# Optimization experiments

Measured on AMD Instinct MI355X. Metric: run time of the kernel, lower is better.

## Reference

```python
import jax, jax.numpy as jnp
import numpy as np

N_EMBD = 1024
N_HEAD = 16
HEAD_DIM = 64


def setup_inputs() -> dict:
    key = jax.random.key(0)
    ks = jax.random.split(key, 5)
    x = jax.random.normal(ks[0], (4, 2048, N_EMBD), dtype=jnp.float32)
    # qkv_proj: Linear(n_embd, 3*n_embd) -- torch weight is [out, in]
    W_qkv = jax.random.normal(ks[1], (3 * N_EMBD, N_EMBD), dtype=jnp.float32) * 0.02
    b_qkv = jnp.zeros((3 * N_EMBD,), dtype=jnp.float32)
    W_out = jax.random.normal(ks[2], (N_EMBD, N_EMBD), dtype=jnp.float32) * 0.02
    b_out = jnp.zeros((N_EMBD,), dtype=jnp.float32)
    return {"x": x, "W_qkv": W_qkv, "b_qkv": b_qkv, "W_out": W_out, "b_out": b_out}


def reference(x, W_qkv, b_qkv, W_out, b_out):
    B, S, C = x.shape
    scale = 1.0 / np.sqrt(HEAD_DIM)
    qkv = jnp.einsum('bsc,oc->bso', x, W_qkv) + b_qkv  # [B,S,3C]
    q, k, v = jnp.split(qkv, 3, axis=-1)
    # [B,S,C] -> [B,H,S,Dh]
    def to_heads(t):
        return t.reshape(B, S, N_HEAD, HEAD_DIM).transpose(0, 2, 1, 3)
    q, k, v = to_heads(q), to_heads(k), to_heads(v)
    scores = jnp.einsum('bhqd,bhkd->bhqk', q, k) * scale  # [B,H,S,S]
    causal = jnp.tril(jnp.ones((S, S), dtype=bool))
    scores = jnp.where(causal[None, None], scores, -jnp.inf)
    weights = jax.nn.softmax(scores.astype(jnp.float32), axis=-1).astype(q.dtype)
    y = jnp.einsum('bhqk,bhkd->bhqd', weights, v)  # [B,H,S,Dh]
    y = y.transpose(0, 2, 1, 3).reshape(B, S, C)
    return jnp.einsum('bsc,oc->bso', y, W_out) + b_out
```

## Files before the change

### kernel.cpp

```cpp
#include <hip/hip_runtime.h>
#include <stdint.h>
#include <stddef.h>

typedef __attribute__((ext_vector_type(8))) short short8;
typedef __attribute__((ext_vector_type(4))) float f32x4;
typedef __attribute__((ext_vector_type(16))) float f32x16;
typedef __attribute__((ext_vector_type(4))) unsigned short ushort4v;
typedef __attribute__((ext_vector_type(4))) unsigned int uint4v;

#define SEQ   2048
#define NH    16
#define BATCH 4
#define GK    1024

__device__ __forceinline__ unsigned short f2bf(float f) {
  union { float f; unsigned int u; } v; v.f = f;
  unsigned int u = v.u;
  u += 0x7fffu + ((u >> 16) & 1u);
  return (unsigned short)(u >> 16);
}

__device__ __forceinline__ unsigned cvtpk_bf16(float lo, float hi) {
  unsigned r;
  asm("v_cvt_pk_bf16_f32 %0, %1, %2" : "=v"(r) : "v"(lo), "v"(hi));
  return r;
}

__device__ __forceinline__ void plswap(unsigned &x, unsigned &y) {
#if __has_builtin(__builtin_amdgcn_permlane32_swap)
  auto r = __builtin_amdgcn_permlane32_swap((int)x, (int)y, false, false);
  x = (unsigned)r[0]; y = (unsigned)r[1];
#else
  const unsigned sx = (unsigned)__shfl_xor((int)x, 32);
  const unsigned sy = (unsigned)__shfl_xor((int)y, 32);
  const bool hi = (threadIdx.x & 63) >= 32;
  const unsigned nx = hi ? sy : x;
  const unsigned ny = hi ? y : sx;
  x = nx; y = ny;
#endif
}

__device__ __forceinline__ void gload16(const unsigned short* g, unsigned short* l) {
  __builtin_amdgcn_global_load_lds(
      (const __attribute__((address_space(1))) unsigned int*)g,
      (__attribute__((address_space(3))) unsigned int*)l, 16, 0, 0);
}

__global__ void cvt_bf16(const float* __restrict__ src, unsigned short* __restrict__ dst, int n4) {
  int i = blockIdx.x * blockDim.x + threadIdx.x;
  const int stride = gridDim.x * blockDim.x;
  for (; i < n4; i += stride) {
    const float4 v = reinterpret_cast<const float4*>(src)[i];
    ushort4v o;
    o[0] = f2bf(v.x); o[1] = f2bf(v.y); o[2] = f2bf(v.z); o[3] = f2bf(v.w);
    reinterpret_cast<ushort4v*>(dst)[i] = o;
  }
}

template<int MODE>
__global__ __launch_bounds__(256, 2)
void gemm_bt(const unsigned short* __restrict__ A,
             const unsigned short* __restrict__ Bw,
             const float* __restrict__ bias,
             unsigned short* __restrict__ q_ws,
             unsigned short* __restrict__ k_ws,
             unsigned short* __restrict__ v_ws,
             float* __restrict__ fout,
             int N)
{
  __shared__ __attribute__((aligned(16))) unsigned short As[128 * 64];
  __shared__ __attribute__((aligned(16))) unsigned short Bs[128 * 64];

  const int t = threadIdx.x;
  const int w = t >> 6, lane = t & 63;
  const int g = lane >> 4, c = lane & 15;
  const int wrow = w >> 1, wcol = w & 1;
  const int m0 = blockIdx.y * 128;
  const int n0 = blockIdx.x * 128;

  const int r8 = lane >> 3;
  const int cgs = (lane & 7) ^ r8;

  const f32x4 fz = {0.f, 0.f, 0.f, 0.f};
  f32x4 acc[4][4];
#pragma unroll
  for (int i = 0; i < 4; ++i)
#pragma unroll
    for (int j = 0; j < 4; ++j) acc[i][j] = fz;

  for (int ks = 0; ks < GK; ks += 64) {
    __syncthreads();
#pragma unroll
    for (int i = 0; i < 4; ++i) {
      const int RB = (i * 4 + w) * 8;
      gload16(A + (size_t)(m0 + RB + r8) * GK + ks + cgs * 8, &As[RB * 64]);
      gload16(Bw + (size_t)(n0 + RB + r8) * GK + ks + cgs * 8, &Bs[RB * 64]);
    }
    __syncthreads();
#pragma unroll
    for (int kk = 0; kk < 2; ++kk) {
      short8 af[4], bfr[4];
#pragma unroll
      for (int mi = 0; mi < 4; ++mi) {
        const int row = wrow * 64 + mi * 16 + c;
        af[mi] = *reinterpret_cast<const short8*>(&As[row * 64 + (((kk * 4 + g) ^ (row & 7)) << 3)]);
      }
#pragma unroll
      for (int ni = 0; ni < 4; ++ni) {
        const int row = wcol * 64 + ni * 16 + c;
        bfr[ni] = *reinterpret_cast<const short8*>(&Bs[row * 64 + (((kk * 4 + g) ^ (row & 7)) << 3)]);
      }
#pragma unroll
      for (int mi = 0; mi < 4; ++mi)
#pragma unroll
        for (int ni = 0; ni < 4; ++ni)
          acc[mi][ni] = __builtin_amdgcn_mfma_f32_16x16x32_bf16(af[mi], bfr[ni], acc[mi][ni], 0, 0, 0);
    }
  }

  if (MODE == 0) {
    const int sec = n0 >> 10;
    unsigned short* dst = (sec == 0) ? q_ws : ((sec == 1) ? k_ws : v_ws);
    const float qsc = (sec == 0) ? (0.125f * 1.44269504f) : 1.0f;
#pragma unroll
    for (int ni = 0; ni < 4; ++ni) {
      const int n = n0 + wcol * 64 + ni * 16 + c;
      const float bb = bias[n];
      const int hh = (n & 1023) >> 6;
      const int d = n & 63;
#pragma unroll
      for (int mi = 0; mi < 4; ++mi) {
#pragma unroll
        for (int r = 0; r < 4; ++r) {
          const int m = m0 + wrow * 64 + mi * 16 + g * 4 + r;
          const int b = m >> 11, s = m & 2047;
          const float val = (acc[mi][ni][r] + bb) * qsc;
          dst[((size_t)((b * NH + hh) * SEQ + s) << 6) + d] = f2bf(val);
        }
      }
    }
  } else {
#pragma unroll
    for (int ni = 0; ni < 4; ++ni) {
      const int n = n0 + wcol * 64 + ni * 16 + c;
      const float bb = bias[n];
#pragma unroll
      for (int mi = 0; mi < 4; ++mi) {
#pragma unroll
        for (int r = 0; r < 4; ++r) {
          const int m = m0 + wrow * 64 + mi * 16 + g * 4 + r;
          fout[(size_t)m * N + n] = acc[mi][ni][r] + bb;
        }
      }
    }
  }
}

__global__ __launch_bounds__(256)
void transpose_v(const unsigned short* __restrict__ v, unsigned short* __restrict__ vt) {
  __shared__ unsigned short T[64][72];
  const int t = threadIdx.x;
  const int bh = blockIdx.y, s0 = blockIdx.x * 64;
  const unsigned short* src = v + ((size_t)bh * SEQ + s0) * 64;
#pragma unroll
  for (int rep = 0; rep < 2; ++rep) {
    const int u = rep * 256 + t;
    const int sr = u >> 3, cg = u & 7;
    const short8 x = *reinterpret_cast<const short8*>(src + (size_t)sr * 64 + cg * 8);
    *reinterpret_cast<short8*>(&T[sr][cg * 8]) = x;
  }
  __syncthreads();
  unsigned short* dst = vt + (size_t)bh * 64 * SEQ + s0;
#pragma unroll
  for (int rep = 0; rep < 2; ++rep) {
    const int u = rep * 256 + t;
    const int d = u >> 3, sc8 = u & 7;
    short8 x;
#pragma unroll
    for (int j = 0; j < 8; ++j) x[j] = (short)T[sc8 * 8 + j][d];
    *reinterpret_cast<short8*>(dst + (size_t)d * SEQ + sc8 * 8) = x;
  }
}

__global__ __launch_bounds__(512, 4)
void attn_fwd4(const unsigned short* __restrict__ q_ws,
               const unsigned short* __restrict__ k_ws,
               const unsigned short* __restrict__ vt_ws,
               unsigned short* __restrict__ y_ws)
{
  __shared__ __attribute__((aligned(16))) unsigned short Ks[2][64 * 64];
  __shared__ __attribute__((aligned(16))) unsigned short Vs[2][64 * 64];

  const int t = threadIdx.x;
  const int w = t >> 6, lane = t & 63;
  const int ql = lane & 31, hi = lane >> 5;
  const int bh = blockIdx.y, b = bh >> 4, h = bh & 15;
  const int jt = (blockIdx.y >= 32) ? (7 - (int)blockIdx.x) : (int)blockIdx.x;
  const int wq0 = jt * 256 + w * 32;
  const int nkt = 4 * jt + 4;

  const int s_row = t >> 3, s_cg = t & 7;
  const int so = s_row * 64 + ((s_cg ^ (s_row & 7)) << 3);

  const unsigned short* kbase = k_ws + (size_t)bh * SEQ * 64;
  const unsigned short* vbase = vt_ws + (size_t)bh * 64 * SEQ;

  short8 rk, rv;
  auto stage_issue = [&](int kt) {
    rk = *reinterpret_cast<const short8*>(kbase + (size_t)kt * 4096 + s_row * 64 + s_cg * 8);
    rv = *reinterpret_cast<const short8*>(vbase + (size_t)s_row * SEQ + kt * 64 + s_cg * 8);
  };
  auto stage_write = [&](int bi) {
    *reinterpret_cast<short8*>(&Ks[bi][so]) = rk;
    *reinterpret_cast<short8*>(&Vs[bi][so]) = rv;
  };

  const unsigned short* qr = q_ws + ((size_t)bh * SEQ + (wq0 + ql)) * 64;
  short8 qf[4];
#pragma unroll
  for (int ks = 0; ks < 4; ++ks)
    qf[ks] = *reinterpret_cast<const short8*>(qr + ks * 16 + hi * 8);

  f32x16 o0, o1;
#pragma unroll
  for (int i = 0; i < 16; ++i) { o0[i] = 0.f; o1[i] = 0.f; }
  float m_run = -1e30f, lsum = 0.f;

  stage_issue(0);
  stage_write(0);

#pragma unroll 1
  for (int kt = 0; kt < nkt; ++kt) {
    const bool more = (kt + 1) < nkt;
    if (more) stage_issue(kt + 1);
    __syncthreads();
    const int cur = kt & 1;
    const int kt64 = kt * 64;

    if (kt64 <= wq0 + 31) {
      short8 kfl[4], kfh[4];
#pragma unroll
      for (int ks = 0; ks < 4; ++ks) {
        kfl[ks] = *reinterpret_cast<const short8*>(
            &Ks[cur][ql * 64 + (((2 * ks + hi) ^ (ql & 7)) << 3)]);
        kfh[ks] = *reinterpret_cast<const short8*>(
            &Ks[cur][(32 + ql) * 64 + (((2 * ks + hi) ^ (ql & 7)) << 3)]);
      }
      f32x16 s0, s1;
#pragma unroll
      for (int i = 0; i < 16; ++i) { s0[i] = 0.f; s1[i] = 0.f; }
      __builtin_amdgcn_s_setprio(1);
#pragma unroll
      for (int ks = 0; ks < 4; ++ks) {
        s0 = __builtin_amdgcn_mfma_f32_32x32x16_bf16(kfl[ks], qf[ks], s0, 0, 0, 0);
        s1 = __builtin_amdgcn_mfma_f32_32x32x16_bf16(kfh[ks], qf[ks], s1, 0, 0, 0);
      }
      __builtin_amdgcn_s_setprio(0);
      if (kt64 + 63 > wq0) {
        const int gq = wq0 + ql;
#pragma unroll
        for (int r = 0; r < 16; ++r) {
          const int krow = (r & 3) + 8 * (r >> 2) + 4 * hi;
          if (kt64 + krow > gq)      s0[r] = -1e30f;
          if (kt64 + 32 + krow > gq) s1[r] = -1e30f;
        }
      }
      float tm = -1e30f;
#pragma unroll
      for (int r = 0; r < 16; ++r) tm = fmaxf(tm, fmaxf(s0[r], s1[r]));
      tm = fmaxf(tm, __shfl_xor(tm, 32));
      if (__any(tm > m_run + 10.0f)) {
        const float m_new = fmaxf(m_run, tm);
        const float al = __builtin_amdgcn_exp2f(m_run - m_new);
        m_run = m_new;
        lsum *= al;
#pragma unroll
        for (int r = 0; r < 16; ++r) {
          const int qq = (r & 3) + 8 * (r >> 2) + 4 * hi;
          const float ar = __shfl(al, qq);
          o0[r] *= ar; o1[r] *= ar;
        }
      }
      float psum = 0.f;
      unsigned W[16];
#pragma unroll
      for (int half = 0; half < 2; ++half) {
#pragma unroll
        for (int gr = 0; gr < 4; ++gr) {
          const float v0 = (half ? s1[gr * 4 + 0] : s0[gr * 4 + 0]) - m_run;
          const float v1 = (half ? s1[gr * 4 + 1] : s0[gr * 4 + 1]) - m_run;
          const float v2 = (half ? s1[gr * 4 + 2] : s0[gr * 4 + 2]) - m_run;
          const float v3 = (half ? s1[gr * 4 + 3] : s0[gr * 4 + 3]) - m_run;
          const float p0 = __builtin_amdgcn_exp2f(v0);
          const float p1 = __builtin_amdgcn_exp2f(v1);
          const float p2 = __builtin_amdgcn_exp2f(v2);
          const float p3 = __builtin_amdgcn_exp2f(v3);
          psum += (p0 + p1) + (p2 + p3);
          W[half * 8 + 2 * gr]     = cvtpk_bf16(p0, p1);
          W[half * 8 + 2 * gr + 1] = cvtpk_bf16(p2, p3);
        }
      }
      lsum += psum;
      short8 pa[4];
#pragma unroll
      for (int q4 = 0; q4 < 4; ++q4) {
        unsigned a0 = W[q4 * 4 + 0], a1 = W[q4 * 4 + 2];
        unsigned b0 = W[q4 * 4 + 1], b1 = W[q4 * 4 + 3];
        plswap(a0, a1);
        plswap(b0, b1);
        uint4v pk; pk[0] = a0; pk[1] = b0; pk[2] = a1; pk[3] = b1;
        pa[q4] = __builtin_bit_cast(short8, pk);
      }
      __builtin_amdgcn_s_setprio(1);
#pragma unroll
      for (int ks = 0; ks < 4; ++ks) {
        const short8 vfl = *reinterpret_cast<const short8*>(
            &Vs[cur][ql * 64 + (((2 * ks + hi) ^ (ql & 7)) << 3)]);
        const short8 vfh = *reinterpret_cast<const short8*>(
            &Vs[cur][(32 + ql) * 64 + (((2 * ks + hi) ^ (ql & 7)) << 3)]);
        o0 = __builtin_amdgcn_mfma_f32_32x32x16_bf16(pa[ks], vfl, o0, 0, 0, 0);
        o1 = __builtin_amdgcn_mfma_f32_32x32x16_bf16(pa[ks], vfh, o1, 0, 0, 0);
      }
      __builtin_amdgcn_s_setprio(0);
    }
    if (more) stage_write((kt + 1) & 1);
  }

  lsum += __shfl_xor(lsum, 32);
  const float linv = 1.f / lsum;
#pragma unroll
  for (int r = 0; r < 16; ++r) {
    const int qq = (r & 3) + 8 * (r >> 2) + 4 * hi;
    const float lr = __shfl(linv, qq);
    const size_t rowo = ((size_t)b * SEQ + (wq0 + qq)) * 1024 + h * 64;
    y_ws[rowo + ql]      = f2bf(o0[r] * lr);
    y_ws[rowo + 32 + ql] = f2bf(o1[r] * lr);
  }
}

extern "C" void kernel_launch(void* const* d_in, const int* in_sizes, int n_in,
                              void* d_out, int out_size, void* d_ws, size_t ws_size,
                              hipStream_t stream)
{
  (void)in_sizes; (void)n_in; (void)out_size; (void)ws_size;
  const float* x     = (const float*)d_in[0];
  const float* W_qkv = (const float*)d_in[1];
  const float* b_qkv = (const float*)d_in[2];
  const float* W_out = (const float*)d_in[3];
  const float* b_out = (const float*)d_in[4];
  float* out = (float*)d_out;

  unsigned short* ws      = (unsigned short*)d_ws;
  unsigned short* x_bf    = ws;
  unsigned short* wqkv_bf = x_bf    + (size_t)8192 * 1024;
  unsigned short* wout_bf = wqkv_bf + (size_t)3072 * 1024;
  unsigned short* q_ws    = wout_bf + (size_t)1024 * 1024;
  unsigned short* k_ws    = q_ws    + (size_t)64 * SEQ * 64;
  unsigned short* v_ws    = k_ws    + (size_t)64 * SEQ * 64;
  unsigned short* y_ws    = v_ws    + (size_t)64 * SEQ * 64;
  unsigned short* vt_ws   = x_bf;

  cvt_bf16<<<2048, 256, 0, stream>>>(x,     x_bf,    (8192 * 1024) / 4);
  cvt_bf16<<<1024, 256, 0, stream>>>(W_qkv, wqkv_bf, (3072 * 1024) / 4);
  cvt_bf16<<<512,  256, 0, stream>>>(W_out, wout_bf, (1024 * 1024) / 4);

  gemm_bt<0><<<dim3(24, 64), 256, 0, stream>>>(x_bf, wqkv_bf, b_qkv, q_ws, k_ws, v_ws, nullptr, 3072);
  transpose_v<<<dim3(SEQ / 64, 64), 256, 0, stream>>>(v_ws, vt_ws);
  attn_fwd4<<<dim3(8, 64), 512, 0, stream>>>(q_ws, k_ws, vt_ws, y_ws);
  gemm_bt<1><<<dim3(8, 64), 256, 0, stream>>>(y_ws, wout_bf, b_out, nullptr, nullptr, nullptr, out, 1024);
}
```

Before: 180.9 us.

## Software-pipeline attention PV with QK, async LDS loads, fuse conversions

The attention kernel now stages K/V tiles with direct global-to-LDS loads and triple-buffers V. It also defers each tile's P·V MFMA to the next iteration so it overlaps with the following QK^T and softmax, with a tail step after the loop. The three fp32-to-bf16 conversion launches are merged into one kernel, and the GEMM launch bound is raised to three blocks per CU. The goals are to hide LDS staging latency, improve MFMA/VALU overlap and cut launch overhead, at the cost of more LDS, register pressure from the GEMM occupancy hint, and branchier conversion code.

```diff
diff --git a/kernel.cpp b/kernel.cpp
--- a/kernel.cpp
+++ b/kernel.cpp
@@ -46,11 +46,16 @@
       (__attribute__((address_space(3))) unsigned int*)l, 16, 0, 0);
 }
 
-__global__ void cvt_bf16(const float* __restrict__ src, unsigned short* __restrict__ dst, int n4) {
+__global__ void cvt_all(const float* __restrict__ x, const float* __restrict__ wqkv,
+                        const float* __restrict__ wout, unsigned short* __restrict__ dst) {
+  const int N1 = (8192 * 1024) / 4, N2 = (3072 * 1024) / 4, N3 = (1024 * 1024) / 4;
   int i = blockIdx.x * blockDim.x + threadIdx.x;
   const int stride = gridDim.x * blockDim.x;
-  for (; i < n4; i += stride) {
-    const float4 v = reinterpret_cast<const float4*>(src)[i];
+  for (; i < N1 + N2 + N3; i += stride) {
+    float4 v;
+    if (i < N1)            v = reinterpret_cast<const float4*>(x)[i];
+    else if (i < N1 + N2)  v = reinterpret_cast<const float4*>(wqkv)[i - N1];
+    else                   v = reinterpret_cast<const float4*>(wout)[i - N1 - N2];
     ushort4v o;
     o[0] = f2bf(v.x); o[1] = f2bf(v.y); o[2] = f2bf(v.z); o[3] = f2bf(v.w);
     reinterpret_cast<ushort4v*>(dst)[i] = o;
@@ -58,7 +63,7 @@
 }
 
 template<int MODE>
-__global__ __launch_bounds__(256, 2)
+__global__ __launch_bounds__(256, 3)
 void gemm_bt(const unsigned short* __restrict__ A,
              const unsigned short* __restrict__ Bw,
              const float* __restrict__ bias,
@@ -183,13 +188,13 @@
 }
 
 __global__ __launch_bounds__(512, 4)
-void attn_fwd4(const unsigned short* __restrict__ q_ws,
+void attn_fwd6(const unsigned short* __restrict__ q_ws,
                const unsigned short* __restrict__ k_ws,
                const unsigned short* __restrict__ vt_ws,
                unsigned short* __restrict__ y_ws)
 {
   __shared__ __attribute__((aligned(16))) unsigned short Ks[2][64 * 64];
-  __shared__ __attribute__((aligned(16))) unsigned short Vs[2][64 * 64];
+  __shared__ __attribute__((aligned(16))) unsigned short Vs[3][64 * 64];
 
   const int t = threadIdx.x;
   const int w = t >> 6, lane = t & 63;
@@ -199,20 +204,15 @@
   const int wq0 = jt * 256 + w * 32;
   const int nkt = 4 * jt + 4;
 
-  const int s_row = t >> 3, s_cg = t & 7;
-  const int so = s_row * 64 + ((s_cg ^ (s_row & 7)) << 3);
+  const int s_row = t >> 3;
+  const int s_swz = (t & 7) ^ (s_row & 7);
 
   const unsigned short* kbase = k_ws + (size_t)bh * SEQ * 64;
   const unsigned short* vbase = vt_ws + (size_t)bh * 64 * SEQ;
 
-  short8 rk, rv;
-  auto stage_issue = [&](int kt) {
-    rk = *reinterpret_cast<const short8*>(kbase + (size_t)kt * 4096 + s_row * 64 + s_cg * 8);
-    rv = *reinterpret_cast<const short8*>(vbase + (size_t)s_row * SEQ + kt * 64 + s_cg * 8);
-  };
-  auto stage_write = [&](int bi) {
-    *reinterpret_cast<short8*>(&Ks[bi][so]) = rk;
-    *reinterpret_cast<short8*>(&Vs[bi][so]) = rv;
+  auto stage = [&](int kt, int kb, int vb) {
+    gload16(kbase + (size_t)kt * 4096 + s_row * 64 + s_swz * 8, &Ks[kb][w * 512]);
+    gload16(vbase + (size_t)s_row * SEQ + kt * 64 + s_swz * 8, &Vs[vb][w * 512]);
   };
 
   const unsigned short* qr = q_ws + ((size_t)bh * SEQ + (wq0 + ql)) * 64;
@@ -225,37 +225,50 @@
 #pragma unroll
   for (int i = 0; i < 16; ++i) { o0[i] = 0.f; o1[i] = 0.f; }
   float m_run = -1e30f, lsum = 0.f;
-
-  stage_issue(0);
-  stage_write(0);
+  short8 pa[4];
+
+  stage(0, 0, 0);
 
 #pragma unroll 1
   for (int kt = 0; kt < nkt; ++kt) {
-    const bool more = (kt + 1) < nkt;
-    if (more) stage_issue(kt + 1);
     __syncthreads();
+    if (kt + 1 < nkt) stage(kt + 1, (kt + 1) & 1, (kt + 1) % 3);
     const int cur = kt & 1;
+    const int pvb = (kt + 2) % 3;
     const int kt64 = kt * 64;
-
-    if (kt64 <= wq0 + 31) {
-      short8 kfl[4], kfh[4];
-#pragma unroll
-      for (int ks = 0; ks < 4; ++ks) {
-        kfl[ks] = *reinterpret_cast<const short8*>(
-            &Ks[cur][ql * 64 + (((2 * ks + hi) ^ (ql & 7)) << 3)]);
-        kfh[ks] = *reinterpret_cast<const short8*>(
-            &Ks[cur][(32 + ql) * 64 + (((2 * ks + hi) ^ (ql & 7)) << 3)]);
-      }
-      f32x16 s0, s1;
+    const bool act  = (kt64 <= wq0 + 31);
+    const bool actp = (kt > 0) && (kt64 - 64 <= wq0 + 31);
+
+    f32x16 s0, s1;
+    if (act) {
 #pragma unroll
       for (int i = 0; i < 16; ++i) { s0[i] = 0.f; s1[i] = 0.f; }
       __builtin_amdgcn_s_setprio(1);
 #pragma unroll
       for (int ks = 0; ks < 4; ++ks) {
-        s0 = __builtin_amdgcn_mfma_f32_32x32x16_bf16(kfl[ks], qf[ks], s0, 0, 0, 0);
-        s1 = __builtin_amdgcn_mfma_f32_32x32x16_bf16(kfh[ks], qf[ks], s1, 0, 0, 0);
+        const short8 kfl = *reinterpret_cast<const short8*>(
+            &Ks[cur][ql * 64 + (((2 * ks + hi) ^ (ql & 7)) << 3)]);
+        const short8 kfh = *reinterpret_cast<const short8*>(
+            &Ks[cur][(32 + ql) * 64 + (((2 * ks + hi) ^ (ql & 7)) << 3)]);
+        s0 = __builtin_amdgcn_mfma_f32_32x32x16_bf16(kfl, qf[ks], s0, 0, 0, 0);
+        s1 = __builtin_amdgcn_mfma_f32_32x32x16_bf16(kfh, qf[ks], s1, 0, 0, 0);
       }
       __builtin_amdgcn_s_setprio(0);
+    }
+    if (actp) {
+      __builtin_amdgcn_s_setprio(1);
+#pragma unroll
+      for (int ks = 0; ks < 4; ++ks) {
+        const short8 vfl = *reinterpret_cast<const short8*>(
+            &Vs[pvb][ql * 64 + (((2 * ks + hi) ^ (ql & 7)) << 3)]);
+        const short8 vfh = *reinterpret_cast<const short8*>(
+            &Vs[pvb][(32 + ql) * 64 + (((2 * ks + hi) ^ (ql & 7)) << 3)]);
+        o0 = __builtin_amdgcn_mfma_f32_32x32x16_bf16(pa[ks], vfl, o0, 0, 0, 0);
+        o1 = __builtin_amdgcn_mfma_f32_32x32x16_bf16(pa[ks], vfh, o1, 0, 0, 0);
+      }
+      __builtin_amdgcn_s_setprio(0);
+    }
+    if (act) {
       if (kt64 + 63 > wq0) {
         const int gq = wq0 + ql;
 #pragma unroll
@@ -301,7 +314,6 @@
         }
       }
       lsum += psum;
-      short8 pa[4];
 #pragma unroll
       for (int q4 = 0; q4 < 4; ++q4) {
         unsigned a0 = W[q4 * 4 + 0], a1 = W[q4 * 4 + 2];
@@ -311,19 +323,22 @@
         uint4v pk; pk[0] = a0; pk[1] = b0; pk[2] = a1; pk[3] = b1;
         pa[q4] = __builtin_bit_cast(short8, pk);
       }
-      __builtin_amdgcn_s_setprio(1);
-#pragma unroll
-      for (int ks = 0; ks < 4; ++ks) {
-        const short8 vfl = *reinterpret_cast<const short8*>(
-            &Vs[cur][ql * 64 + (((2 * ks + hi) ^ (ql & 7)) << 3)]);
-        const short8 vfh = *reinterpret_cast<const short8*>(
-            &Vs[cur][(32 + ql) * 64 + (((2 * ks + hi) ^ (ql & 7)) << 3)]);
-        o0 = __builtin_amdgcn_mfma_f32_32x32x16_bf16(pa[ks], vfl, o0, 0, 0, 0);
-        o1 = __builtin_amdgcn_mfma_f32_32x32x16_bf16(pa[ks], vfh, o1, 0, 0, 0);
-      }
-      __builtin_amdgcn_s_setprio(0);
-    }
-    if (more) stage_write((kt + 1) & 1);
+    }
+  }
+
+  if ((nkt - 1) * 64 <= wq0 + 31) {
+    const int pvb = (nkt - 1) % 3;
+    __builtin_amdgcn_s_setprio(1);
+#pragma unroll
+    for (int ks = 0; ks < 4; ++ks) {
+      const short8 vfl = *reinterpret_cast<const short8*>(
+          &Vs[pvb][ql * 64 + (((2 * ks + hi) ^ (ql & 7)) << 3)]);
+      const short8 vfh = *reinterpret_cast<const short8*>(
+          &Vs[pvb][(32 + ql) * 64 + (((2 * ks + hi) ^ (ql & 7)) << 3)]);
+      o0 = __builtin_amdgcn_mfma_f32_32x32x16_bf16(pa[ks], vfl, o0, 0, 0, 0);
+      o1 = __builtin_amdgcn_mfma_f32_32x32x16_bf16(pa[ks], vfh, o1, 0, 0, 0);
+    }
+    __builtin_amdgcn_s_setprio(0);
   }
 
   lsum += __shfl_xor(lsum, 32);
@@ -360,12 +375,10 @@
   unsigned short* y_ws    = v_ws    + (size_t)64 * SEQ * 64;
   unsigned short* vt_ws   = x_bf;
 
-  cvt_bf16<<<2048, 256, 0, stream>>>(x,     x_bf,    (8192 * 1024) / 4);
-  cvt_bf16<<<1024, 256, 0, stream>>>(W_qkv, wqkv_bf, (3072 * 1024) / 4);
-  cvt_bf16<<<512,  256, 0, stream>>>(W_out, wout_bf, (1024 * 1024) / 4);
+  cvt_all<<<2048, 256, 0, stream>>>(x, W_qkv, W_out, x_bf);
 
   gemm_bt<0><<<dim3(24, 64), 256, 0, stream>>>(x_bf, wqkv_bf, b_qkv, q_ws, k_ws, v_ws, nullptr, 3072);
   transpose_v<<<dim3(SEQ / 64, 64), 256, 0, stream>>>(v_ws, vt_ws);
-  attn_fwd4<<<dim3(8, 64), 512, 0, stream>>>(q_ws, k_ws, vt_ws, y_ws);
+  attn_fwd6<<<dim3(8, 64), 512, 0, stream>>>(q_ws, k_ws, vt_ws, y_ws);
   gemm_bt<1><<<dim3(8, 64), 256, 0, stream>>>(y_ws, wout_bf, b_out, nullptr, nullptr, nullptr, out, 1024);
 }
```

Result: no change. 183.3 us (+1.3%).

## Merge bf16 conversions and add pipelined 256x128 QKV GEMM kernel

Applied to the files above, without the earlier changes.

Merges the three fp32-to-bf16 conversion launches into one kernel covering x and both weights. Replaces the QKV projection GEMM with a 512-thread, 256x128-tile kernel that keeps three LDS buffers, loads two k-steps ahead, interleaves staging with MFMA phases under barriers and s_setprio, and remaps blocks for L2 locality. The output GEMM becomes its own kernel with a higher occupancy hint. This aims to cut launch overhead and hide global load latency in the largest GEMM, at the cost of more LDS per block and many barriers.

```diff
diff --git a/kernel.cpp b/kernel.cpp
--- a/kernel.cpp
+++ b/kernel.cpp
@@ -46,27 +46,169 @@
       (__attribute__((address_space(3))) unsigned int*)l, 16, 0, 0);
 }
 
-__global__ void cvt_bf16(const float* __restrict__ src, unsigned short* __restrict__ dst, int n4) {
+__global__ void cvt_all(const float* __restrict__ x, const float* __restrict__ wqkv,
+                        const float* __restrict__ wout, unsigned short* __restrict__ dst) {
+  const int N1 = (8192 * 1024) / 4, N2 = (3072 * 1024) / 4, N3 = (1024 * 1024) / 4;
   int i = blockIdx.x * blockDim.x + threadIdx.x;
   const int stride = gridDim.x * blockDim.x;
-  for (; i < n4; i += stride) {
-    const float4 v = reinterpret_cast<const float4*>(src)[i];
+  for (; i < N1 + N2 + N3; i += stride) {
+    float4 v;
+    if (i < N1)            v = reinterpret_cast<const float4*>(x)[i];
+    else if (i < N1 + N2)  v = reinterpret_cast<const float4*>(wqkv)[i - N1];
+    else                   v = reinterpret_cast<const float4*>(wout)[i - N1 - N2];
     ushort4v o;
     o[0] = f2bf(v.x); o[1] = f2bf(v.y); o[2] = f2bf(v.z); o[3] = f2bf(v.w);
     reinterpret_cast<ushort4v*>(dst)[i] = o;
   }
 }
 
-template<int MODE>
-__global__ __launch_bounds__(256, 2)
-void gemm_bt(const unsigned short* __restrict__ A,
-             const unsigned short* __restrict__ Bw,
-             const float* __restrict__ bias,
-             unsigned short* __restrict__ q_ws,
-             unsigned short* __restrict__ k_ws,
-             unsigned short* __restrict__ v_ws,
-             float* __restrict__ fout,
-             int N)
+__global__ __launch_bounds__(512, 2)
+void gemm_qkv8(const unsigned short* __restrict__ A,
+               const unsigned short* __restrict__ Bw,
+               const float* __restrict__ bias,
+               unsigned short* __restrict__ q_ws,
+               unsigned short* __restrict__ k_ws,
+               unsigned short* __restrict__ v_ws)
+{
+  __shared__ __attribute__((aligned(16))) unsigned short As[3][256 * 64];
+  __shared__ __attribute__((aligned(16))) unsigned short Bs[3][128 * 64];
+
+  const int t = threadIdx.x;
+  const int w = t >> 6, lane = t & 63;
+  const int g = lane >> 4, c = lane & 15;
+  const int wrow = w >> 1, wcol = w & 1;
+
+  const int l = (int)blockIdx.x;
+  const int tau = (l & 7) * 96 + (l >> 3);
+  const int m0 = (tau / 24) * 256;
+  const int n0 = (tau % 24) * 128;
+
+  const int w8r = w * 8 + (lane >> 3);
+  const int cgs = (lane & 7) ^ (lane >> 3);
+
+  auto stageA2 = [&](int kt, int buf, int r0) {
+#pragma unroll
+    for (int r = r0; r < r0 + 2; ++r)
+      gload16(A + (size_t)(m0 + r * 64 + w8r) * GK + kt * 64 + cgs * 8,
+              &As[buf][(r * 64 + w * 8) * 64]);
+  };
+  auto stageB2 = [&](int kt, int buf) {
+#pragma unroll
+    for (int r = 0; r < 2; ++r)
+      gload16(Bw + (size_t)(n0 + r * 64 + w8r) * GK + kt * 64 + cgs * 8,
+              &Bs[buf][(r * 64 + w * 8) * 64]);
+  };
+
+  auto rdA = [&](int buf, int mi, int kk) -> short8 {
+    const int row = wrow * 64 + mi * 16 + c;
+    return *reinterpret_cast<const short8*>(&As[buf][row * 64 + (((kk * 4 + g) ^ (row & 7)) << 3)]);
+  };
+  auto rdB = [&](int buf, int ni, int kk) -> short8 {
+    const int row = wcol * 64 + ni * 16 + c;
+    return *reinterpret_cast<const short8*>(&Bs[buf][row * 64 + (((kk * 4 + g) ^ (row & 7)) << 3)]);
+  };
+
+  const f32x4 fz = {0.f, 0.f, 0.f, 0.f};
+  f32x4 acc[4][4];
+#pragma unroll
+  for (int i = 0; i < 4; ++i)
+#pragma unroll
+    for (int j = 0; j < 4; ++j) acc[i][j] = fz;
+
+  stageA2(0, 0, 0); stageA2(0, 0, 2); stageB2(0, 0);
+  stageA2(1, 1, 0); stageA2(1, 1, 2); stageB2(1, 1);
+
+#pragma unroll 1
+  for (int ks = 0; ks < 16; ++ks) {
+    const int buf = ks % 3;
+    const int sb  = (ks + 2) % 3;
+    const bool st = (ks + 2) < 16;
+
+    if (ks < 15) asm volatile("s_waitcnt vmcnt(6)" ::: "memory");
+    else         asm volatile("s_waitcnt vmcnt(0)" ::: "memory");
+    __builtin_amdgcn_s_barrier();
+
+    short8 b0[4], a0, a1;
+#pragma unroll
+    for (int ni = 0; ni < 4; ++ni) b0[ni] = rdB(buf, ni, 0);
+    a0 = rdA(buf, 0, 0); a1 = rdA(buf, 1, 0);
+    if (st) stageA2(ks + 2, sb, 0);
+    __builtin_amdgcn_s_barrier();
+    __builtin_amdgcn_s_setprio(1);
+#pragma unroll
+    for (int ni = 0; ni < 4; ++ni) {
+      acc[0][ni] = __builtin_amdgcn_mfma_f32_16x16x32_bf16(a0, b0[ni], acc[0][ni], 0, 0, 0);
+      acc[1][ni] = __builtin_amdgcn_mfma_f32_16x16x32_bf16(a1, b0[ni], acc[1][ni], 0, 0, 0);
+    }
+    __builtin_amdgcn_s_setprio(0);
+    __builtin_amdgcn_s_barrier();
+
+    a0 = rdA(buf, 2, 0); a1 = rdA(buf, 3, 0);
+    if (st) stageA2(ks + 2, sb, 2);
+    __builtin_amdgcn_s_barrier();
+    __builtin_amdgcn_s_setprio(1);
+#pragma unroll
+    for (int ni = 0; ni < 4; ++ni) {
+      acc[2][ni] = __builtin_amdgcn_mfma_f32_16x16x32_bf16(a0, b0[ni], acc[2][ni], 0, 0, 0);
+      acc[3][ni] = __builtin_amdgcn_mfma_f32_16x16x32_bf16(a1, b0[ni], acc[3][ni], 0, 0, 0);
+    }
+    __builtin_amdgcn_s_setprio(0);
+    __builtin_amdgcn_s_barrier();
+
+#pragma unroll
+    for (int ni = 0; ni < 4; ++ni) b0[ni] = rdB(buf, ni, 1);
+    a0 = rdA(buf, 0, 1); a1 = rdA(buf, 1, 1);
+    if (st) stageB2(ks + 2, sb);
+    __builtin_amdgcn_s_barrier();
+    __builtin_amdgcn_s_setprio(1);
+#pragma unroll
+    for (int ni = 0; ni < 4; ++ni) {
+      acc[0][ni] = __builtin_amdgcn_mfma_f32_16x16x32_bf16(a0, b0[ni], acc[0][ni], 0, 0, 0);
+      acc[1][ni] = __builtin_amdgcn_mfma_f32_16x16x32_bf16(a1, b0[ni], acc[1][ni], 0, 0, 0);
+    }
+    __builtin_amdgcn_s_setprio(0);
+    __builtin_amdgcn_s_barrier();
+
+    a0 = rdA(buf, 2, 1); a1 = rdA(buf, 3, 1);
+    __builtin_amdgcn_s_barrier();
+    __builtin_amdgcn_s_setprio(1);
+#pragma unroll
+    for (int ni = 0; ni < 4; ++ni) {
+      acc[2][ni] = __builtin_amdgcn_mfma_f32_16x16x32_bf16(a0, b0[ni], acc[2][ni], 0, 0, 0);
+      acc[3][ni] = __builtin_amdgcn_mfma_f32_16x16x32_bf16(a1, b0[ni], acc[3][ni], 0, 0, 0);
+    }
+    __builtin_amdgcn_s_setprio(0);
+    __builtin_amdgcn_s_barrier();
+  }
+
+  const int sec = n0 >> 10;
+  unsigned short* dst = (sec == 0) ? q_ws : ((sec == 1) ? k_ws : v_ws);
+  const float qsc = (sec == 0) ? (0.125f * 1.44269504f) : 1.0f;
+#pragma unroll
+  for (int ni = 0; ni < 4; ++ni) {
+    const int n = n0 + wcol * 64 + ni * 16 + c;
+    const float bb = bias[n];
+    const int hh = (n & 1023) >> 6;
+    const int d = n & 63;
+#pragma unroll
+    for (int mi = 0; mi < 4; ++mi) {
+#pragma unroll
+      for (int r = 0; r < 4; ++r) {
+        const int m = m0 + wrow * 64 + mi * 16 + g * 4 + r;
+        const int b = m >> 11, s = m & 2047;
+        const float val = (acc[mi][ni][r] + bb) * qsc;
+        dst[((size_t)((b * NH + hh) * SEQ + s) << 6) + d] = f2bf(val);
+      }
+    }
+  }
+}
+
+__global__ __launch_bounds__(256, 3)
+void gemm_out(const unsigned short* __restrict__ A,
+              const unsigned short* __restrict__ Bw,
+              const float* __restrict__ bias,
+              float* __restrict__ fout,
+              int N)
 {
   __shared__ __attribute__((aligned(16))) unsigned short As[128 * 64];
   __shared__ __attribute__((aligned(16))) unsigned short Bs[128 * 64];
@@ -118,39 +260,16 @@
     }
   }
 
-  if (MODE == 0) {
-    const int sec = n0 >> 10;
-    unsigned short* dst = (sec == 0) ? q_ws : ((sec == 1) ? k_ws : v_ws);
-    const float qsc = (sec == 0) ? (0.125f * 1.44269504f) : 1.0f;
-#pragma unroll
-    for (int ni = 0; ni < 4; ++ni) {
-      const int n = n0 + wcol * 64 + ni * 16 + c;
-      const float bb = bias[n];
-      const int hh = (n & 1023) >> 6;
-      const int d = n & 63;
-#pragma unroll
-      for (int mi = 0; mi < 4; ++mi) {
-#pragma unroll
-        for (int r = 0; r < 4; ++r) {
-          const int m = m0 + wrow * 64 + mi * 16 + g * 4 + r;
-          const int b = m >> 11, s = m & 2047;
-          const float val = (acc[mi][ni][r] + bb) * qsc;
-          dst[((size_t)((b * NH + hh) * SEQ + s) << 6) + d] = f2bf(val);
-        }
-      }
-    }
-  } else {
-#pragma unroll
-    for (int ni = 0; ni < 4; ++ni) {
-      const int n = n0 + wcol * 64 + ni * 16 + c;
-      const float bb = bias[n];
-#pragma unroll
-      for (int mi = 0; mi < 4; ++mi) {
-#pragma unroll
-        for (int r = 0; r < 4; ++r) {
-          const int m = m0 + wrow * 64 + mi * 16 + g * 4 + r;
-          fout[(size_t)m * N + n] = acc[mi][ni][r] + bb;
-        }
+#pragma unroll
+  for (int ni = 0; ni < 4; ++ni) {
+    const int n = n0 + wcol * 64 + ni * 16 + c;
+    const float bb = bias[n];
+#pragma unroll
+    for (int mi = 0; mi < 4; ++mi) {
+#pragma unroll
+      for (int r = 0; r < 4; ++r) {
+        const int m = m0 + wrow * 64 + mi * 16 + g * 4 + r;
+        fout[(size_t)m * N + n] = acc[mi][ni][r] + bb;
       }
     }
   }
@@ -183,7 +302,7 @@
 }
 
 __global__ __launch_bounds__(512, 4)
-void attn_fwd4(const unsigned short* __restrict__ q_ws,
+void attn_fwd8(const unsigned short* __restrict__ q_ws,
                const unsigned short* __restrict__ k_ws,
                const unsigned short* __restrict__ vt_ws,
                unsigned short* __restrict__ y_ws)
@@ -360,12 +479,10 @@
   unsigned short* y_ws    = v_ws    + (size_t)64 * SEQ * 64;
   unsigned short* vt_ws   = x_bf;
 
-  cvt_bf16<<<2048, 256, 0, stream>>>(x,     x_bf,    (8192 * 1024) / 4);
-  cvt_bf16<<<1024, 256, 0, stream>>>(W_qkv, wqkv_bf, (3072 * 1024) / 4);
-  cvt_bf16<<<512,  256, 0, stream>>>(W_out, wout_bf, (1024 * 1024) / 4);
-
-  gemm_bt<0><<<dim3(24, 64), 256, 0, stream>>>(x_bf, wqkv_bf, b_qkv, q_ws, k_ws, v_ws, nullptr, 3072);
+  cvt_all<<<2048, 256, 0, stream>>>(x, W_qkv, W_out, x_bf);
+
+  gemm_qkv8<<<768, 512, 0, stream>>>(x_bf, wqkv_bf, b_qkv, q_ws, k_ws, v_ws);
   transpose_v<<<dim3(SEQ / 64, 64), 256, 0, stream>>>(v_ws, vt_ws);
-  attn_fwd4<<<dim3(8, 64), 512, 0, stream>>>(q_ws, k_ws, vt_ws, y_ws);
-  gemm_bt<1><<<dim3(8, 64), 256, 0, stream>>>(y_ws, wout_bf, b_out, nullptr, nullptr, nullptr, out, 1024);
-}
+  attn_fwd8<<<dim3(8, 64), 512, 0, stream>>>(q_ws, k_ws, vt_ws, y_ws);
+  gemm_out<<<dim3(8, 64), 256, 0, stream>>>(y_ws, wout_bf, b_out, out, 1024);
+}
```

Result: slower. 187.9 us (median of 2 runs) (+3.9%).

## Triple-buffer attention K/V via direct LDS loads, fuse conversions, raise GEMM occupancy

Applied to the files above, without the earlier changes.

The attention kernel now stages K and V with global_load_lds straight into a three-deep shared-memory ring. It uses manual vmcnt waits and a raw barrier instead of register staging plus __syncthreads, so loads run two tiles ahead of compute. The three fp32-to-bf16 conversion launches are merged into one kernel to cut launch overhead. The GEMM launch bounds are raised to ask for three blocks per CU. The risks are more LDS per attention block and register pressure in the GEMM, plus the correctness of the hand-written waitcnt sequencing.

```diff
diff --git a/kernel.cpp b/kernel.cpp
--- a/kernel.cpp
+++ b/kernel.cpp
@@ -46,11 +46,16 @@
       (__attribute__((address_space(3))) unsigned int*)l, 16, 0, 0);
 }
 
-__global__ void cvt_bf16(const float* __restrict__ src, unsigned short* __restrict__ dst, int n4) {
+__global__ void cvt_all(const float* __restrict__ x, const float* __restrict__ wqkv,
+                        const float* __restrict__ wout, unsigned short* __restrict__ dst) {
+  const int N1 = (8192 * 1024) / 4, N2 = (3072 * 1024) / 4, N3 = (1024 * 1024) / 4;
   int i = blockIdx.x * blockDim.x + threadIdx.x;
   const int stride = gridDim.x * blockDim.x;
-  for (; i < n4; i += stride) {
-    const float4 v = reinterpret_cast<const float4*>(src)[i];
+  for (; i < N1 + N2 + N3; i += stride) {
+    float4 v;
+    if (i < N1)            v = reinterpret_cast<const float4*>(x)[i];
+    else if (i < N1 + N2)  v = reinterpret_cast<const float4*>(wqkv)[i - N1];
+    else                   v = reinterpret_cast<const float4*>(wout)[i - N1 - N2];
     ushort4v o;
     o[0] = f2bf(v.x); o[1] = f2bf(v.y); o[2] = f2bf(v.z); o[3] = f2bf(v.w);
     reinterpret_cast<ushort4v*>(dst)[i] = o;
@@ -58,7 +63,7 @@
 }
 
 template<int MODE>
-__global__ __launch_bounds__(256, 2)
+__global__ __launch_bounds__(256, 3)
 void gemm_bt(const unsigned short* __restrict__ A,
              const unsigned short* __restrict__ Bw,
              const float* __restrict__ bias,
@@ -183,13 +188,13 @@
 }
 
 __global__ __launch_bounds__(512, 4)
-void attn_fwd4(const unsigned short* __restrict__ q_ws,
-               const unsigned short* __restrict__ k_ws,
-               const unsigned short* __restrict__ vt_ws,
-               unsigned short* __restrict__ y_ws)
+void attn_fwd10(const unsigned short* __restrict__ q_ws,
+                const unsigned short* __restrict__ k_ws,
+                const unsigned short* __restrict__ vt_ws,
+                unsigned short* __restrict__ y_ws)
 {
-  __shared__ __attribute__((aligned(16))) unsigned short Ks[2][64 * 64];
-  __shared__ __attribute__((aligned(16))) unsigned short Vs[2][64 * 64];
+  __shared__ __attribute__((aligned(16))) unsigned short Ks[3][64 * 64];
+  __shared__ __attribute__((aligned(16))) unsigned short Vs[3][64 * 64];
 
   const int t = threadIdx.x;
   const int w = t >> 6, lane = t & 63;
@@ -199,20 +204,15 @@
   const int wq0 = jt * 256 + w * 32;
   const int nkt = 4 * jt + 4;
 
-  const int s_row = t >> 3, s_cg = t & 7;
-  const int so = s_row * 64 + ((s_cg ^ (s_row & 7)) << 3);
+  const int s_row = t >> 3;
+  const int s_swz = (t & 7) ^ (s_row & 7);
 
   const unsigned short* kbase = k_ws + (size_t)bh * SEQ * 64;
   const unsigned short* vbase = vt_ws + (size_t)bh * 64 * SEQ;
 
-  short8 rk, rv;
-  auto stage_issue = [&](int kt) {
-    rk = *reinterpret_cast<const short8*>(kbase + (size_t)kt * 4096 + s_row * 64 + s_cg * 8);
-    rv = *reinterpret_cast<const short8*>(vbase + (size_t)s_row * SEQ + kt * 64 + s_cg * 8);
-  };
-  auto stage_write = [&](int bi) {
-    *reinterpret_cast<short8*>(&Ks[bi][so]) = rk;
-    *reinterpret_cast<short8*>(&Vs[bi][so]) = rv;
+  auto stage = [&](int kt, int bi) {
+    gload16(kbase + (size_t)kt * 4096 + s_row * 64 + s_swz * 8, &Ks[bi][w * 512]);
+    gload16(vbase + (size_t)s_row * SEQ + kt * 64 + s_swz * 8, &Vs[bi][w * 512]);
   };
 
   const unsigned short* qr = q_ws + ((size_t)bh * SEQ + (wq0 + ql)) * 64;
@@ -226,15 +226,18 @@
   for (int i = 0; i < 16; ++i) { o0[i] = 0.f; o1[i] = 0.f; }
   float m_run = -1e30f, lsum = 0.f;
 
-  stage_issue(0);
-  stage_write(0);
+  stage(0, 0);
+  stage(1, 1);
 
 #pragma unroll 1
   for (int kt = 0; kt < nkt; ++kt) {
-    const bool more = (kt + 1) < nkt;
-    if (more) stage_issue(kt + 1);
-    __syncthreads();
-    const int cur = kt & 1;
+    if (kt + 1 < nkt) asm volatile("s_waitcnt lgkmcnt(0) vmcnt(2)" ::: "memory");
+    else              asm volatile("s_waitcnt lgkmcnt(0) vmcnt(0)" ::: "memory");
+    asm volatile("s_barrier" ::: "memory");
+    __builtin_amdgcn_sched_barrier(0);
+    if (kt + 2 < nkt) stage(kt + 2, (kt + 2) % 3);
+
+    const int cur = kt % 3;
     const int kt64 = kt * 64;
 
     if (kt64 <= wq0 + 31) {
@@ -323,7 +326,6 @@
       }
       __builtin_amdgcn_s_setprio(0);
     }
-    if (more) stage_write((kt + 1) & 1);
   }
 
   lsum += __shfl_xor(lsum, 32);
@@ -360,12 +362,10 @@
   unsigned short* y_ws    = v_ws    + (size_t)64 * SEQ * 64;
   unsigned short* vt_ws   = x_bf;
 
-  cvt_bf16<<<2048, 256, 0, stream>>>(x,     x_bf,    (8192 * 1024) / 4);
-  cvt_bf16<<<1024, 256, 0, stream>>>(W_qkv, wqkv_bf, (3072 * 1024) / 4);
-  cvt_bf16<<<512,  256, 0, stream>>>(W_out, wout_bf, (1024 * 1024) / 4);
+  cvt_all<<<2048, 256, 0, stream>>>(x, W_qkv, W_out, x_bf);
 
   gemm_bt<0><<<dim3(24, 64), 256, 0, stream>>>(x_bf, wqkv_bf, b_qkv, q_ws, k_ws, v_ws, nullptr, 3072);
   transpose_v<<<dim3(SEQ / 64, 64), 256, 0, stream>>>(v_ws, vt_ws);
-  attn_fwd4<<<dim3(8, 64), 512, 0, stream>>>(q_ws, k_ws, vt_ws, y_ws);
+  attn_fwd10<<<dim3(8, 64), 512, 0, stream>>>(q_ws, k_ws, vt_ws, y_ws);
   gemm_bt<1><<<dim3(8, 64), 256, 0, stream>>>(y_ws, wout_bf, b_out, nullptr, nullptr, nullptr, out, 1024);
 }
```

Result: no change. 181.8 us (+0.5%).
